# Optimization experiments

Hardware: AMD Instinct MI355X
Metric: run time of the kernel (lower is better)

## Reference

```python
import jax, jax.numpy as jnp
import numpy as np

N, E, F_IN, HID, HEADS, OUT = 50000, 600000, 128, 128, 8, 64
C = HID // HEADS  # per-head channels = 16
NEG_SLOPE = 0.2


def _gat_layer(x, ei_src, ei_dst, Wl, bl, Ws, Wd, a_s, a_d, bc):
    n = x.shape[0]
    lin_out = x @ Wl + bl                              # [N, HID]
    xs = (x @ Ws).reshape(n, HEADS, C)                 # [N, H, C] (lin_src, no bias)
    xd = (x @ Wd).reshape(n, HEADS, C)                 # [N, H, C] (lin_dst, no bias)
    alpha_s = jnp.sum(xs * a_s, axis=-1)               # [N, H]
    alpha_d = jnp.sum(xd * a_d, axis=-1)               # [N, H]
    e = jax.nn.leaky_relu(alpha_s[ei_src] + alpha_d[ei_dst], NEG_SLOPE)  # [E, H]
    # segment softmax over destination nodes
    m = jax.lax.stop_gradient(jax.ops.segment_max(e, ei_dst, num_segments=n))
    p = jnp.exp(e - m[ei_dst])
    denom = jax.ops.segment_sum(p, ei_dst, num_segments=n)
    alpha = p / (denom[ei_dst] + 1e-16)                # [E, H]
    msg = alpha[:, :, None] * xs[ei_src]               # [E, H, C]
    agg = jax.ops.segment_sum(msg, ei_dst, num_segments=n).reshape(n, HID) + bc
    # eval mode: attention/feature dropout are identity
    return jax.nn.elu(lin_out + agg)


def setup_inputs() -> dict:
    key = jax.random.key(0)
    ks = jax.random.split(key, 20)
    s = 0.05
    d = {
        "x": jax.random.normal(ks[0], (N, F_IN), jnp.float32),
        "edge_index": jax.random.randint(ks[1], (2, E), 0, N, jnp.int64)
        if jax.config.jax_enable_x64 else jax.random.randint(ks[1], (2, E), 0, N, jnp.int32),
    }
    dims_in = [F_IN, HID]
    for l in range(2):
        di = dims_in[l]
        d[f"W_lin{l}"] = jax.random.normal(ks[2 + 8 * l], (di, HID), jnp.float32) * s
        d[f"b_lin{l}"] = jnp.zeros((HID,), jnp.float32)
        d[f"W_src{l}"] = jax.random.normal(ks[3 + 8 * l], (di, HID), jnp.float32) * s
        d[f"W_dst{l}"] = jax.random.normal(ks[4 + 8 * l], (di, HID), jnp.float32) * s
        d[f"att_src{l}"] = jax.random.normal(ks[5 + 8 * l], (HEADS, C), jnp.float32) * s
        d[f"att_dst{l}"] = jax.random.normal(ks[6 + 8 * l], (HEADS, C), jnp.float32) * s
        d[f"b_conv{l}"] = jnp.zeros((HID,), jnp.float32)
    d["W_out"] = jax.random.normal(ks[18], (HID, OUT), jnp.float32) * s
    d["b_out"] = jnp.zeros((OUT,), jnp.float32)
    return d


def reference(x, edge_index,
              W_lin0, b_lin0, W_src0, W_dst0, att_src0, att_dst0, b_conv0,
              W_lin1, b_lin1, W_src1, W_dst1, att_src1, att_dst1, b_conv1,
              W_out, b_out):
    ei_src, ei_dst = edge_index[0], edge_index[1]
    h = _gat_layer(x, ei_src, ei_dst, W_lin0, b_lin0, W_src0, W_dst0, att_src0, att_dst0, b_conv0)
    h = _gat_layer(h, ei_src, ei_dst, W_lin1, b_lin1, W_src1, W_dst1, att_src1, att_dst1, b_conv1)
    return h @ W_out + b_out
```

## Files before the change

### kernel.cpp

```cpp
#include <hip/hip_runtime.h>
#include <cstdint>
#include <cstddef>

#define NEG_SLOPE 0.2f

typedef __bf16 bf16x8 __attribute__((ext_vector_type(8)));
typedef float f32x4 __attribute__((ext_vector_type(4)));

static __device__ __forceinline__ unsigned short f2bf(float f) {
  unsigned int u = __float_as_uint(f);
  unsigned int r = (u + 0x7FFFu + ((u >> 16) & 1u)) >> 16;
  return (unsigned short)r;
}
static __device__ __forceinline__ float bf2f(unsigned short u) {
  return __uint_as_float(((unsigned int)u) << 16);
}
static __device__ __forceinline__ float pklo(unsigned int x) {
  return __uint_as_float(x << 16);
}
static __device__ __forceinline__ float pkhi(unsigned int x) {
  return __uint_as_float(x & 0xffff0000u);
}

__global__ void k_degree(const int* __restrict__ ei, int* __restrict__ deg, int E) {
  int e = blockIdx.x * 256 + threadIdx.x;
  if (e < E) atomicAdd(&deg[ei[E + e]], 1);
}

__global__ __launch_bounds__(256) void k_scan_local(const int* __restrict__ deg,
                                                    int* __restrict__ lex,
                                                    int* __restrict__ bsum, int n) {
  __shared__ int ts[256];
  const int t = threadIdx.x;
  const int base = blockIdx.x * 1024 + t * 4;
  int4 d = {0, 0, 0, 0};
  if (base + 3 < n) d = *reinterpret_cast<const int4*>(&deg[base]);
  else {
    if (base + 0 < n) d.x = deg[base + 0];
    if (base + 1 < n) d.y = deg[base + 1];
    if (base + 2 < n) d.z = deg[base + 2];
  }
  int s = d.x + d.y + d.z + d.w;
  ts[t] = s;
  __syncthreads();
  for (int off = 1; off < 256; off <<= 1) {
    int y = (t >= off) ? ts[t - off] : 0;
    __syncthreads();
    ts[t] += y;
    __syncthreads();
  }
  int pre = ts[t] - s;
  int4 o;
  o.x = pre; o.y = pre + d.x; o.z = pre + d.x + d.y; o.w = pre + d.x + d.y + d.z;
  if (base + 3 < n) *reinterpret_cast<int4*>(&lex[base]) = o;
  else {
    if (base + 0 < n) lex[base + 0] = o.x;
    if (base + 1 < n) lex[base + 1] = o.y;
    if (base + 2 < n) lex[base + 2] = o.z;
  }
  if (t == 255) bsum[blockIdx.x] = ts[255];
}

__global__ __launch_bounds__(256) void k_scan_bsum(int* __restrict__ bsum, int nb) {
  __shared__ int ts[256];
  const int t = threadIdx.x;
  int v = (t < nb) ? bsum[t] : 0;
  ts[t] = v;
  __syncthreads();
  for (int off = 1; off < 256; off <<= 1) {
    int y = (t >= off) ? ts[t - off] : 0;
    __syncthreads();
    ts[t] += y;
    __syncthreads();
  }
  if (t < nb) bsum[t] = ts[t] - v;
}

__global__ void k_scan_add(const int* __restrict__ lex, const int* __restrict__ bsum,
                           int* __restrict__ rowptr, int* __restrict__ cursor,
                           int n, int E) {
  int i = blockIdx.x * 256 + threadIdx.x;
  if (i < n) {
    int v = lex[i] + bsum[i >> 10];
    rowptr[i] = v;
    cursor[i] = v;
  }
  if (i == n) rowptr[n] = E;
}

__global__ void k_scatter(const int* __restrict__ ei, int* __restrict__ cursor,
                          unsigned short* __restrict__ col, int E) {
  int e = blockIdx.x * 256 + threadIdx.x;
  if (e >= E) return;
  int d = ei[E + e];
  int pos = atomicAdd(&cursor[d], 1);
  col[pos] = (unsigned short)ei[e];
}

static __device__ __forceinline__ unsigned short pack_wt_elem(
    const float* __restrict__ Wl, const float* __restrict__ Ws,
    const float* __restrict__ Wd, const float* __restrict__ as_,
    const float* __restrict__ ad_, int t) {
  int j = t >> 7, k = t & 127;
  float val;
  if (j < 128) val = Wl[k * 128 + j];
  else if (j < 256) val = Ws[k * 128 + (j - 128)];
  else {
    int jj = j - 256;
    int h = jj & 7;
    const float* W = (jj < 8) ? Ws : Wd;
    const float* a = (jj < 8) ? as_ : ad_;
    float s = 0.f;
#pragma unroll
    for (int c = 0; c < 16; ++c) s += W[k * 128 + h * 16 + c] * a[h * 16 + c];
    val = s;
  }
  return f2bf(val);
}

__global__ void k_pack_all(
    const float* __restrict__ Wl0, const float* __restrict__ Ws0, const float* __restrict__ Wd0,
    const float* __restrict__ as0, const float* __restrict__ ad0,
    const float* __restrict__ Wl1, const float* __restrict__ Ws1, const float* __restrict__ Wd1,
    const float* __restrict__ as1, const float* __restrict__ ad1,
    const float* __restrict__ Wo,
    unsigned short* __restrict__ wt0, unsigned short* __restrict__ wt1,
    unsigned short* __restrict__ wot) {
  const int SZ = 272 * 128;
  int t = blockIdx.x * 256 + threadIdx.x;
  if (t < SZ) {
    wt0[t] = pack_wt_elem(Wl0, Ws0, Wd0, as0, ad0, t);
  } else if (t < 2 * SZ) {
    wt1[t - SZ] = pack_wt_elem(Wl1, Ws1, Wd1, as1, ad1, t - SZ);
  } else if (t < 2 * SZ + 64 * 128) {
    int u = t - 2 * SZ;
    int nn = u >> 7, k = u & 127;
    wot[u] = f2bf(Wo[k * 64 + nn]);
  }
}

template <typename TIN>
__global__ __launch_bounds__(256, 3) void k_gemm_fused(
    const TIN* __restrict__ X, const unsigned short* __restrict__ wt,
    const float* __restrict__ bl, const float* __restrict__ bc,
    unsigned int* __restrict__ ylin_pk, unsigned short* __restrict__ xsb,
    unsigned short* __restrict__ asd_s, unsigned short* __restrict__ asd_d,
    int n) {
  __shared__ __align__(16) unsigned short xa[32][136];
  const int tid = threadIdx.x;
  const int wave = tid >> 6, lane = tid & 63;
  const int lr = lane & 15, lg = lane >> 4;
  const int row0 = blockIdx.x * 32;
  const int f0 = wave * 4;
  const bool w3 = (wave == 3);

  bf16x8 bfr[4][4];
#pragma unroll
  for (int ff = 0; ff < 4; ++ff)
#pragma unroll
    for (int s = 0; s < 4; ++s)
      bfr[ff][s] = *reinterpret_cast<const bf16x8*>(
          &wt[(size_t)((f0 + ff) * 16 + lr) * 128 + s * 32 + lg * 8]);
  bf16x8 bfr4[4];
  if (w3) {
#pragma unroll
    for (int s = 0; s < 4; ++s)
      bfr4[s] = *reinterpret_cast<const bf16x8*>(
          &wt[(size_t)(256 + lr) * 128 + s * 32 + lg * 8]);
  }

  if constexpr (sizeof(TIN) == 4) {
#pragma unroll
    for (int i = 0; i < 4; ++i) {
      int c = tid + i * 256;
      int r = c >> 5, kq = c & 31;
      float4 v = make_float4(0.f, 0.f, 0.f, 0.f);
      if (row0 + r < n)
        v = reinterpret_cast<const float4*>(X)[(size_t)(row0 + r) * 32 + kq];
      ushort4 o;
      o.x = f2bf(v.x); o.y = f2bf(v.y); o.z = f2bf(v.z); o.w = f2bf(v.w);
      *reinterpret_cast<ushort4*>(&xa[r][kq * 4]) = o;
    }
  } else {
#pragma unroll
    for (int i = 0; i < 2; ++i) {
      int c = tid + i * 256;
      int r = c >> 4, ko = c & 15;
      uint4 v = {0u, 0u, 0u, 0u};
      if (row0 + r < n)
        v = reinterpret_cast<const uint4*>(X)[(size_t)(row0 + r) * 16 + ko];
      *reinterpret_cast<uint4*>(&xa[r][ko * 8]) = v;
    }
  }
  __syncthreads();

  f32x4 acc[2][4];
  f32x4 acc4[2];
#pragma unroll
  for (int g = 0; g < 2; ++g) {
    acc4[g] = (f32x4){0.f, 0.f, 0.f, 0.f};
#pragma unroll
    for (int ff = 0; ff < 4; ++ff) acc[g][ff] = (f32x4){0.f, 0.f, 0.f, 0.f};
  }

#pragma unroll
  for (int s = 0; s < 4; ++s) {
    bf16x8 a0 = *reinterpret_cast<const bf16x8*>(&xa[lr][s * 32 + lg * 8]);
    bf16x8 a1 = *reinterpret_cast<const bf16x8*>(&xa[16 + lr][s * 32 + lg * 8]);
#pragma unroll
    for (int ff = 0; ff < 4; ++ff) {
      acc[0][ff] = __builtin_amdgcn_mfma_f32_16x16x32_bf16(a0, bfr[ff][s], acc[0][ff], 0, 0, 0);
      acc[1][ff] = __builtin_amdgcn_mfma_f32_16x16x32_bf16(a1, bfr[ff][s], acc[1][ff], 0, 0, 0);
    }
    if (w3) {
      acc4[0] = __builtin_amdgcn_mfma_f32_16x16x32_bf16(a0, bfr4[s], acc4[0], 0, 0, 0);
      acc4[1] = __builtin_amdgcn_mfma_f32_16x16x32_bf16(a1, bfr4[s], acc4[1], 0, 0, 0);
    }
  }

  if (f0 < 8) {
#pragma unroll
    for (int g = 0; g < 2; ++g)
#pragma unroll
      for (int ff = 0; ff < 4; ++ff) {
        int j = (f0 + ff) * 16 + lr;
        float blc = bl[j] + bc[j];
#pragma unroll
        for (int r = 0; r < 4; ++r) {
          int row = row0 + g * 16 + lg * 4 + r;
          float vb = acc[g][ff][r] + blc;
          float v2 = __shfl(vb, lane ^ 1);
          if (row < n && (lr & 1) == 0)
            ylin_pk[(size_t)row * 64 + (j >> 1)] =
                (unsigned int)f2bf(vb) | ((unsigned int)f2bf(v2) << 16);
        }
      }
  } else {
#pragma unroll
    for (int g = 0; g < 2; ++g)
#pragma unroll
      for (int ff = 0; ff < 4; ++ff) {
        int j = (f0 - 8 + ff) * 16 + lr;
#pragma unroll
        for (int r = 0; r < 4; ++r) {
          int row = row0 + g * 16 + lg * 4 + r;
          if (row < n) xsb[(size_t)row * 128 + j] = f2bf(acc[g][ff][r]);
        }
      }
    if (w3) {
#pragma unroll
      for (int g = 0; g < 2; ++g)
#pragma unroll
        for (int r = 0; r < 4; ++r) {
          int row = row0 + g * 16 + lg * 4 + r;
          if (row < n) {
            unsigned short v = f2bf(acc4[g][r]);
            if (lr < 8) asd_s[(size_t)row * 8 + lr] = v;
            else        asd_d[(size_t)row * 8 + (lr - 8)] = v;
          }
        }
    }
  }
}

__global__ __launch_bounds__(256) void k_gemm_out(
    const unsigned short* __restrict__ X, const unsigned short* __restrict__ wo,
    const float* __restrict__ bias, float* __restrict__ out, int n) {
  __shared__ __align__(16) unsigned short xa[64][136];
  __shared__ __align__(16) unsigned short ws[64][136];
  const int tid = threadIdx.x;
  const int row0 = blockIdx.x * 64;

#pragma unroll
  for (int i = 0; i < 4; ++i) {
    int c = tid + i * 256;
    int r = c >> 4, ko = c & 15;
    uint4 v = {0u, 0u, 0u, 0u};
    if (row0 + r < n)
      v = reinterpret_cast<const uint4*>(X)[(size_t)(row0 + r) * 16 + ko];
    *reinterpret_cast<uint4*>(&xa[r][ko * 8]) = v;
  }
#pragma unroll
  for (int i = 0; i < 4; ++i) {
    int c = tid + i * 256;
    int r = c >> 4, ko = c & 15;
    *reinterpret_cast<uint4*>(&ws[r][ko * 8]) =
        reinterpret_cast<const uint4*>(wo)[(size_t)r * 16 + ko];
  }
  __syncthreads();

  const int w = tid >> 6, lane = tid & 63;
  const int lr = lane & 15, lg = lane >> 4;
  f32x4 acc[4];
#pragma unroll
  for (int f = 0; f < 4; ++f) acc[f] = (f32x4){0.f, 0.f, 0.f, 0.f};

#pragma unroll
  for (int s = 0; s < 4; ++s) {
    bf16x8 a = *reinterpret_cast<const bf16x8*>(&xa[w * 16 + lr][s * 32 + lg * 8]);
#pragma unroll
    for (int f = 0; f < 4; ++f) {
      bf16x8 b = *reinterpret_cast<const bf16x8*>(&ws[f * 16 + lr][s * 32 + lg * 8]);
      acc[f] = __builtin_amdgcn_mfma_f32_16x16x32_bf16(a, b, acc[f], 0, 0, 0);
    }
  }
#pragma unroll
  for (int f = 0; f < 4; ++f) {
#pragma unroll
    for (int r = 0; r < 4; ++r) {
      int row = row0 + w * 16 + lg * 4 + r;
      if (row < n)
        out[(size_t)row * 64 + f * 16 + lr] = acc[f][r] + bias[f * 16 + lr];
    }
  }
}

__global__ __launch_bounds__(256) void k_aggregate(
    const unsigned int* __restrict__ ylin_pk, const unsigned int* __restrict__ xsp,
    const unsigned short* __restrict__ asd_s, const unsigned short* __restrict__ asd_d,
    const int* __restrict__ rowptr, const unsigned short* __restrict__ col,
    unsigned int* __restrict__ hout_pk, int n) {
  int node = (blockIdx.x * blockDim.x + threadIdx.x) >> 6;
  if (node >= n) return;
  const int lane = threadIdx.x & 63;
  const int el = lane >> 3;
  const int hh = lane & 7;
  const int hb4 = (lane >> 3) << 2;
  const int beg = rowptr[node], end = rowptr[node + 1];

  const float ad_hh = bf2f(asd_d[(size_t)node * 8 + hh]);

  float dsum = 0.f, acc0 = 0.f, acc1 = 0.f;
  int ebase = beg;
  for (; ebase + 8 < end; ebase += 16) {
    int eA = ebase + el;
    int eB = ebase + 8 + el;
    bool vB = eB < end;
    int esB = vB ? eB : (end - 1);
    int srcA = (int)__builtin_nontemporal_load(&col[eA]);
    int srcB = (int)__builtin_nontemporal_load(&col[esB]);
    float svA = bf2f(asd_s[(size_t)srcA * 8 + hh]) + ad_hh;
    float svB = bf2f(asd_s[(size_t)srcB * 8 + hh]) + ad_hh;
    svA = fmaxf(svA, NEG_SLOPE * svA);
    svB = fmaxf(svB, NEG_SLOPE * svB);
    float peA = __expf(svA);
    float peB = vB ? __expf(svB) : 0.f;
#pragma unroll
    for (int q = 0; q < 8; ++q) {
      float pq = __uint_as_float(__builtin_amdgcn_ds_bpermute(
          q * 32 + hb4, __float_as_uint(peA)));
      int sq = __builtin_amdgcn_readlane(srcA, q * 8);
      unsigned int xv = xsp[(size_t)sq * 64 + lane];
      dsum += pq;
      acc0 += pq * pklo(xv);
      acc1 += pq * pkhi(xv);
    }
#pragma unroll
    for (int q = 0; q < 8; ++q) {
      float pq = __uint_as_float(__builtin_amdgcn_ds_bpermute(
          q * 32 + hb4, __float_as_uint(peB)));
      int sq = __builtin_amdgcn_readlane(srcB, q * 8);
      unsigned int xv = xsp[(size_t)sq * 64 + lane];
      dsum += pq;
      acc0 += pq * pklo(xv);
      acc1 += pq * pkhi(xv);
    }
  }
  for (; ebase < end; ebase += 8) {
    int e1 = ebase + el;
    bool valid = e1 < end;
    int esafe = valid ? e1 : (end - 1);
    int srcp = (int)__builtin_nontemporal_load(&col[esafe]);
    float sv = bf2f(asd_s[(size_t)srcp * 8 + hh]) + ad_hh;
    sv = fmaxf(sv, NEG_SLOPE * sv);
    float pe = valid ? __expf(sv) : 0.f;
#pragma unroll
    for (int q = 0; q < 8; ++q) {
      float pq = __uint_as_float(__builtin_amdgcn_ds_bpermute(
          q * 32 + hb4, __float_as_uint(pe)));
      int sq = __builtin_amdgcn_readlane(srcp, q * 8);
      unsigned int xv = xsp[(size_t)sq * 64 + lane];
      dsum += pq;
      acc0 += pq * pklo(xv);
      acc1 += pq * pkhi(xv);
    }
  }
  float inv = 1.f / (dsum + 1e-16f);
  unsigned int y = __builtin_nontemporal_load(&ylin_pk[(size_t)node * 64 + lane]);
  float l0 = pklo(y) + acc0 * inv;
  float l1 = pkhi(y) + acc1 * inv;
  l0 = l0 > 0.f ? l0 : __expf(l0) - 1.f;
  l1 = l1 > 0.f ? l1 : __expf(l1) - 1.f;
  hout_pk[(size_t)node * 64 + lane] =
      (unsigned int)f2bf(l0) | ((unsigned int)f2bf(l1) << 16);
}

extern "C" void kernel_launch(void* const* d_in, const int* in_sizes, int n_in,
                              void* d_out, int out_size, void* d_ws, size_t ws_size,
                              hipStream_t stream) {
  const float* x      = (const float*)d_in[0];
  const int*   ei     = (const int*)d_in[1];
  const float* W_lin0 = (const float*)d_in[2];
  const float* b_lin0 = (const float*)d_in[3];
  const float* W_src0 = (const float*)d_in[4];
  const float* W_dst0 = (const float*)d_in[5];
  const float* att_s0 = (const float*)d_in[6];
  const float* att_d0 = (const float*)d_in[7];
  const float* b_cnv0 = (const float*)d_in[8];
  const float* W_lin1 = (const float*)d_in[9];
  const float* b_lin1 = (const float*)d_in[10];
  const float* W_src1 = (const float*)d_in[11];
  const float* W_dst1 = (const float*)d_in[12];
  const float* att_s1 = (const float*)d_in[13];
  const float* att_d1 = (const float*)d_in[14];
  const float* b_cnv1 = (const float*)d_in[15];
  const float* W_out  = (const float*)d_in[16];
  const float* b_out  = (const float*)d_in[17];
  float* out = (float*)d_out;

  const int N = in_sizes[0] / 128;
  const int E = in_sizes[1] / 2;
  const int NB = (N + 1023) / 1024;
  const int MB32 = (N + 31) / 32;

  char* p = (char*)d_ws;
  unsigned int* ylin    = (unsigned int*)p;   p += (size_t)N * 64 * 4;
  unsigned short* xsb   = (unsigned short*)p; p += (size_t)N * 128 * 2;
  unsigned short* hb    = (unsigned short*)p; p += (size_t)N * 128 * 2;
  unsigned short* asd_s = (unsigned short*)p; p += (size_t)N * 8 * 2;
  unsigned short* asd_d = (unsigned short*)p; p += (size_t)N * 8 * 2;
  unsigned short* wt0   = (unsigned short*)p; p += (size_t)272 * 128 * 2;
  unsigned short* wt1   = (unsigned short*)p; p += (size_t)272 * 128 * 2;
  unsigned short* wot   = (unsigned short*)p; p += (size_t)64 * 128 * 2;
  int* rowptr = (int*)p;                      p += (size_t)(N + 4) * 4;
  int* cursor = (int*)p;                      p += (size_t)N * 4;
  int* deg    = (int*)p;                      p += (size_t)N * 4;
  int* lex    = (int*)p;                      p += (size_t)N * 4;
  int* bsum   = (int*)p;                      p += (size_t)256 * 4;
  unsigned short* col = (unsigned short*)p;   p += (size_t)E * 2;

  dim3 b256(256);

  hipMemsetAsync(deg, 0, (size_t)N * 4, stream);
  k_degree<<<(E + 255) / 256, b256, 0, stream>>>(ei, deg, E);
  k_scan_local<<<NB, b256, 0, stream>>>(deg, lex, bsum, N);
  k_scan_bsum<<<1, b256, 0, stream>>>(bsum, NB);
  k_scan_add<<<(N + 256) / 256, b256, 0, stream>>>(lex, bsum, rowptr, cursor, N, E);
  k_scatter<<<(E + 255) / 256, b256, 0, stream>>>(ei, cursor, col, E);

  k_pack_all<<<(2 * 272 * 128 + 64 * 128 + 255) / 256, b256, 0, stream>>>(
      W_lin0, W_src0, W_dst0, att_s0, att_d0,
      W_lin1, W_src1, W_dst1, att_s1, att_d1,
      W_out, wt0, wt1, wot);

  for (int layer = 0; layer < 2; ++layer) {
    const float* bl = layer ? b_lin1 : b_lin0;
    const float* bc = layer ? b_cnv1 : b_cnv0;
    const unsigned short* wt = layer ? wt1 : wt0;

    if (layer == 0)
      k_gemm_fused<float><<<MB32, b256, 0, stream>>>(x, wt0, bl, bc, ylin, xsb,
                                                     asd_s, asd_d, N);
    else
      k_gemm_fused<unsigned short><<<MB32, b256, 0, stream>>>(hb, wt, bl, bc, ylin, xsb,
                                                              asd_s, asd_d, N);
    k_aggregate<<<(N + 3) / 4, b256, 0, stream>>>(
        ylin, (const unsigned int*)xsb, asd_s, asd_d, rowptr, col,
        (unsigned int*)hb, N);
  }
  k_gemm_out<<<(N + 63) / 64, b256, 0, stream>>>(hb, wot, b_out, out, N);
}
```

Before: 187.1 us.

## Merge preprocessing kernels and interleave edge scatter with layer-0 GEMM blocks

Weight packing and degree counting are merged into one launch. The CSR scatter is folded into the layer-0 GEMM kernel, with scatter blocks spread evenly among GEMM blocks. This cuts launch count and lets the atomic-bound scatter overlap tensor-core work. The output GEMM now keeps its weights in registers and uses 32-row tiles with no weight LDS staging, and the ylin load in aggregate is issued earlier to hide its latency. Interleaving heterogeneous blocks may hurt occupancy balance, and the scatter's col ordering still depends on atomics.

```diff
diff --git a/kernel.cpp b/kernel.cpp
--- a/kernel.cpp
+++ b/kernel.cpp
@@ -20,11 +20,6 @@
 }
 static __device__ __forceinline__ float pkhi(unsigned int x) {
   return __uint_as_float(x & 0xffff0000u);
-}
-
-__global__ void k_degree(const int* __restrict__ ei, int* __restrict__ deg, int E) {
-  int e = blockIdx.x * 256 + threadIdx.x;
-  if (e < E) atomicAdd(&deg[ei[E + e]], 1);
 }
 
 __global__ __launch_bounds__(256) void k_scan_local(const int* __restrict__ deg,
@@ -86,15 +81,6 @@
     cursor[i] = v;
   }
   if (i == n) rowptr[n] = E;
-}
-
-__global__ void k_scatter(const int* __restrict__ ei, int* __restrict__ cursor,
-                          unsigned short* __restrict__ col, int E) {
-  int e = blockIdx.x * 256 + threadIdx.x;
-  if (e >= E) return;
-  int d = ei[E + e];
-  int pos = atomicAdd(&cursor[d], 1);
-  col[pos] = (unsigned short)ei[e];
 }
 
 static __device__ __forceinline__ unsigned short pack_wt_elem(
@@ -118,30 +104,162 @@
   return f2bf(val);
 }
 
-__global__ void k_pack_all(
+__global__ void k_init(
     const float* __restrict__ Wl0, const float* __restrict__ Ws0, const float* __restrict__ Wd0,
     const float* __restrict__ as0, const float* __restrict__ ad0,
     const float* __restrict__ Wl1, const float* __restrict__ Ws1, const float* __restrict__ Wd1,
     const float* __restrict__ as1, const float* __restrict__ ad1,
     const float* __restrict__ Wo,
     unsigned short* __restrict__ wt0, unsigned short* __restrict__ wt1,
-    unsigned short* __restrict__ wot) {
+    unsigned short* __restrict__ wot,
+    const int* __restrict__ ei, int* __restrict__ deg, int E, int packBlocks) {
   const int SZ = 272 * 128;
-  int t = blockIdx.x * 256 + threadIdx.x;
-  if (t < SZ) {
-    wt0[t] = pack_wt_elem(Wl0, Ws0, Wd0, as0, ad0, t);
-  } else if (t < 2 * SZ) {
-    wt1[t - SZ] = pack_wt_elem(Wl1, Ws1, Wd1, as1, ad1, t - SZ);
-  } else if (t < 2 * SZ + 64 * 128) {
-    int u = t - 2 * SZ;
-    int nn = u >> 7, k = u & 127;
-    wot[u] = f2bf(Wo[k * 64 + nn]);
-  }
-}
-
-template <typename TIN>
-__global__ __launch_bounds__(256, 3) void k_gemm_fused(
-    const TIN* __restrict__ X, const unsigned short* __restrict__ wt,
+  if ((int)blockIdx.x < packBlocks) {
+    int t = blockIdx.x * 256 + threadIdx.x;
+    if (t < SZ) {
+      wt0[t] = pack_wt_elem(Wl0, Ws0, Wd0, as0, ad0, t);
+    } else if (t < 2 * SZ) {
+      wt1[t - SZ] = pack_wt_elem(Wl1, Ws1, Wd1, as1, ad1, t - SZ);
+    } else if (t < 2 * SZ + 64 * 128) {
+      int u = t - 2 * SZ;
+      int nn = u >> 7, k = u & 127;
+      wot[u] = f2bf(Wo[k * 64 + nn]);
+    }
+  } else {
+    int e = (blockIdx.x - packBlocks) * 256 + threadIdx.x;
+    if (e < E) atomicAdd(&deg[ei[E + e]], 1);
+  }
+}
+
+__global__ __launch_bounds__(256, 3) void k_gemm0_scatter(
+    const float* __restrict__ X, const unsigned short* __restrict__ wt,
+    const float* __restrict__ bl, const float* __restrict__ bc,
+    unsigned int* __restrict__ ylin_pk, unsigned short* __restrict__ xsb,
+    unsigned short* __restrict__ asd_s, unsigned short* __restrict__ asd_d,
+    int n, int gemmBlocks,
+    const int* __restrict__ ei, int* __restrict__ cursor,
+    unsigned short* __restrict__ col, int E, int total) {
+  __shared__ __align__(16) unsigned short xa[32][136];
+  const int i = blockIdx.x;
+  const int before = (int)(((long long)i * gemmBlocks) / total);
+  const int after  = (int)(((long long)(i + 1) * gemmBlocks) / total);
+
+  if (after == before) {
+    int e = (i - after) * 256 + threadIdx.x;
+    if (e < E) {
+      int d = ei[E + e];
+      int pos = atomicAdd(&cursor[d], 1);
+      col[pos] = (unsigned short)ei[e];
+    }
+    return;
+  }
+
+  const int tid = threadIdx.x;
+  const int wave = tid >> 6, lane = tid & 63;
+  const int lr = lane & 15, lg = lane >> 4;
+  const int row0 = before * 32;
+  const int f0 = wave * 4;
+  const bool w3 = (wave == 3);
+
+  bf16x8 bfr[4][4];
+#pragma unroll
+  for (int ff = 0; ff < 4; ++ff)
+#pragma unroll
+    for (int s = 0; s < 4; ++s)
+      bfr[ff][s] = *reinterpret_cast<const bf16x8*>(
+          &wt[(size_t)((f0 + ff) * 16 + lr) * 128 + s * 32 + lg * 8]);
+  bf16x8 bfr4[4];
+  if (w3) {
+#pragma unroll
+    for (int s = 0; s < 4; ++s)
+      bfr4[s] = *reinterpret_cast<const bf16x8*>(
+          &wt[(size_t)(256 + lr) * 128 + s * 32 + lg * 8]);
+  }
+
+#pragma unroll
+  for (int ii = 0; ii < 4; ++ii) {
+    int c = tid + ii * 256;
+    int r = c >> 5, kq = c & 31;
+    float4 v = make_float4(0.f, 0.f, 0.f, 0.f);
+    if (row0 + r < n)
+      v = reinterpret_cast<const float4*>(X)[(size_t)(row0 + r) * 32 + kq];
+    ushort4 o;
+    o.x = f2bf(v.x); o.y = f2bf(v.y); o.z = f2bf(v.z); o.w = f2bf(v.w);
+    *reinterpret_cast<ushort4*>(&xa[r][kq * 4]) = o;
+  }
+  __syncthreads();
+
+  f32x4 acc[2][4];
+  f32x4 acc4[2];
+#pragma unroll
+  for (int g = 0; g < 2; ++g) {
+    acc4[g] = (f32x4){0.f, 0.f, 0.f, 0.f};
+#pragma unroll
+    for (int ff = 0; ff < 4; ++ff) acc[g][ff] = (f32x4){0.f, 0.f, 0.f, 0.f};
+  }
+
+#pragma unroll
+  for (int s = 0; s < 4; ++s) {
+    bf16x8 a0 = *reinterpret_cast<const bf16x8*>(&xa[lr][s * 32 + lg * 8]);
+    bf16x8 a1 = *reinterpret_cast<const bf16x8*>(&xa[16 + lr][s * 32 + lg * 8]);
+#pragma unroll
+    for (int ff = 0; ff < 4; ++ff) {
+      acc[0][ff] = __builtin_amdgcn_mfma_f32_16x16x32_bf16(a0, bfr[ff][s], acc[0][ff], 0, 0, 0);
+      acc[1][ff] = __builtin_amdgcn_mfma_f32_16x16x32_bf16(a1, bfr[ff][s], acc[1][ff], 0, 0, 0);
+    }
+    if (w3) {
+      acc4[0] = __builtin_amdgcn_mfma_f32_16x16x32_bf16(a0, bfr4[s], acc4[0], 0, 0, 0);
+      acc4[1] = __builtin_amdgcn_mfma_f32_16x16x32_bf16(a1, bfr4[s], acc4[1], 0, 0, 0);
+    }
+  }
+
+  if (f0 < 8) {
+#pragma unroll
+    for (int g = 0; g < 2; ++g)
+#pragma unroll
+      for (int ff = 0; ff < 4; ++ff) {
+        int j = (f0 + ff) * 16 + lr;
+        float blc = bl[j] + bc[j];
+#pragma unroll
+        for (int r = 0; r < 4; ++r) {
+          int row = row0 + g * 16 + lg * 4 + r;
+          float vb = acc[g][ff][r] + blc;
+          float v2 = __shfl(vb, lane ^ 1);
+          if (row < n && (lr & 1) == 0)
+            ylin_pk[(size_t)row * 64 + (j >> 1)] =
+                (unsigned int)f2bf(vb) | ((unsigned int)f2bf(v2) << 16);
+        }
+      }
+  } else {
+#pragma unroll
+    for (int g = 0; g < 2; ++g)
+#pragma unroll
+      for (int ff = 0; ff < 4; ++ff) {
+        int j = (f0 - 8 + ff) * 16 + lr;
+#pragma unroll
+        for (int r = 0; r < 4; ++r) {
+          int row = row0 + g * 16 + lg * 4 + r;
+          if (row < n) xsb[(size_t)row * 128 + j] = f2bf(acc[g][ff][r]);
+        }
+      }
+    if (w3) {
+#pragma unroll
+      for (int g = 0; g < 2; ++g)
+#pragma unroll
+        for (int r = 0; r < 4; ++r) {
+          int row = row0 + g * 16 + lg * 4 + r;
+          if (row < n) {
+            unsigned short v = f2bf(acc4[g][r]);
+            if (lr < 8) asd_s[(size_t)row * 8 + lr] = v;
+            else        asd_d[(size_t)row * 8 + (lr - 8)] = v;
+          }
+        }
+    }
+  }
+}
+
+__global__ __launch_bounds__(256, 3) void k_gemm_fused1(
+    const unsigned short* __restrict__ X, const unsigned short* __restrict__ wt,
     const float* __restrict__ bl, const float* __restrict__ bc,
     unsigned int* __restrict__ ylin_pk, unsigned short* __restrict__ xsb,
     unsigned short* __restrict__ asd_s, unsigned short* __restrict__ asd_d,
@@ -169,28 +287,14 @@
           &wt[(size_t)(256 + lr) * 128 + s * 32 + lg * 8]);
   }
 
-  if constexpr (sizeof(TIN) == 4) {
-#pragma unroll
-    for (int i = 0; i < 4; ++i) {
-      int c = tid + i * 256;
-      int r = c >> 5, kq = c & 31;
-      float4 v = make_float4(0.f, 0.f, 0.f, 0.f);
-      if (row0 + r < n)
-        v = reinterpret_cast<const float4*>(X)[(size_t)(row0 + r) * 32 + kq];
-      ushort4 o;
-      o.x = f2bf(v.x); o.y = f2bf(v.y); o.z = f2bf(v.z); o.w = f2bf(v.w);
-      *reinterpret_cast<ushort4*>(&xa[r][kq * 4]) = o;
-    }
-  } else {
-#pragma unroll
-    for (int i = 0; i < 2; ++i) {
-      int c = tid + i * 256;
-      int r = c >> 4, ko = c & 15;
-      uint4 v = {0u, 0u, 0u, 0u};
-      if (row0 + r < n)
-        v = reinterpret_cast<const uint4*>(X)[(size_t)(row0 + r) * 16 + ko];
-      *reinterpret_cast<uint4*>(&xa[r][ko * 8]) = v;
-    }
+#pragma unroll
+  for (int i = 0; i < 2; ++i) {
+    int c = tid + i * 256;
+    int r = c >> 4, ko = c & 15;
+    uint4 v = {0u, 0u, 0u, 0u};
+    if (row0 + r < n)
+      v = reinterpret_cast<const uint4*>(X)[(size_t)(row0 + r) * 16 + ko];
+    *reinterpret_cast<uint4*>(&xa[r][ko * 8]) = v;
   }
   __syncthreads();
 
@@ -263,16 +367,23 @@
   }
 }
 
-__global__ __launch_bounds__(256) void k_gemm_out(
-    const unsigned short* __restrict__ X, const unsigned short* __restrict__ wo,
+__global__ __launch_bounds__(256, 3) void k_gemm_out(
+    const unsigned short* __restrict__ X, const unsigned short* __restrict__ wot,
     const float* __restrict__ bias, float* __restrict__ out, int n) {
-  __shared__ __align__(16) unsigned short xa[64][136];
-  __shared__ __align__(16) unsigned short ws[64][136];
+  __shared__ __align__(16) unsigned short xa[32][136];
   const int tid = threadIdx.x;
-  const int row0 = blockIdx.x * 64;
-
-#pragma unroll
-  for (int i = 0; i < 4; ++i) {
+  const int wave = tid >> 6, lane = tid & 63;
+  const int lr = lane & 15, lg = lane >> 4;
+  const int row0 = blockIdx.x * 32;
+
+  bf16x8 bo[4];
+#pragma unroll
+  for (int s = 0; s < 4; ++s)
+    bo[s] = *reinterpret_cast<const bf16x8*>(
+        &wot[(size_t)(wave * 16 + lr) * 128 + s * 32 + lg * 8]);
+
+#pragma unroll
+  for (int i = 0; i < 2; ++i) {
     int c = tid + i * 256;
     int r = c >> 4, ko = c & 15;
     uint4 v = {0u, 0u, 0u, 0u};
@@ -280,39 +391,26 @@
       v = reinterpret_cast<const uint4*>(X)[(size_t)(row0 + r) * 16 + ko];
     *reinterpret_cast<uint4*>(&xa[r][ko * 8]) = v;
   }
-#pragma unroll
-  for (int i = 0; i < 4; ++i) {
-    int c = tid + i * 256;
-    int r = c >> 4, ko = c & 15;
-    *reinterpret_cast<uint4*>(&ws[r][ko * 8]) =
-        reinterpret_cast<const uint4*>(wo)[(size_t)r * 16 + ko];
-  }
   __syncthreads();
 
-  const int w = tid >> 6, lane = tid & 63;
-  const int lr = lane & 15, lg = lane >> 4;
-  f32x4 acc[4];
-#pragma unroll
-  for (int f = 0; f < 4; ++f) acc[f] = (f32x4){0.f, 0.f, 0.f, 0.f};
-
+  f32x4 acc[2];
+  acc[0] = (f32x4){0.f, 0.f, 0.f, 0.f};
+  acc[1] = (f32x4){0.f, 0.f, 0.f, 0.f};
 #pragma unroll
   for (int s = 0; s < 4; ++s) {
-    bf16x8 a = *reinterpret_cast<const bf16x8*>(&xa[w * 16 + lr][s * 32 + lg * 8]);
-#pragma unroll
-    for (int f = 0; f < 4; ++f) {
-      bf16x8 b = *reinterpret_cast<const bf16x8*>(&ws[f * 16 + lr][s * 32 + lg * 8]);
-      acc[f] = __builtin_amdgcn_mfma_f32_16x16x32_bf16(a, b, acc[f], 0, 0, 0);
-    }
-  }
-#pragma unroll
-  for (int f = 0; f < 4; ++f) {
+    bf16x8 a0 = *reinterpret_cast<const bf16x8*>(&xa[lr][s * 32 + lg * 8]);
+    bf16x8 a1 = *reinterpret_cast<const bf16x8*>(&xa[16 + lr][s * 32 + lg * 8]);
+    acc[0] = __builtin_amdgcn_mfma_f32_16x16x32_bf16(a0, bo[s], acc[0], 0, 0, 0);
+    acc[1] = __builtin_amdgcn_mfma_f32_16x16x32_bf16(a1, bo[s], acc[1], 0, 0, 0);
+  }
+  float bv = bias[wave * 16 + lr];
+#pragma unroll
+  for (int g = 0; g < 2; ++g)
 #pragma unroll
     for (int r = 0; r < 4; ++r) {
-      int row = row0 + w * 16 + lg * 4 + r;
-      if (row < n)
-        out[(size_t)row * 64 + f * 16 + lr] = acc[f][r] + bias[f * 16 + lr];
-    }
-  }
+      int row = row0 + g * 16 + lg * 4 + r;
+      if (row < n) out[(size_t)row * 64 + wave * 16 + lr] = acc[g][r] + bv;
+    }
 }
 
 __global__ __launch_bounds__(256) void k_aggregate(
@@ -329,6 +427,7 @@
   const int beg = rowptr[node], end = rowptr[node + 1];
 
   const float ad_hh = bf2f(asd_d[(size_t)node * 8 + hh]);
+  unsigned int y = __builtin_nontemporal_load(&ylin_pk[(size_t)node * 64 + lane]);
 
   float dsum = 0.f, acc0 = 0.f, acc1 = 0.f;
   int ebase = beg;
@@ -386,7 +485,6 @@
     }
   }
   float inv = 1.f / (dsum + 1e-16f);
-  unsigned int y = __builtin_nontemporal_load(&ylin_pk[(size_t)node * 64 + lane]);
   float l0 = pklo(y) + acc0 * inv;
   float l1 = pkhi(y) + acc1 * inv;
   l0 = l0 > 0.f ? l0 : __expf(l0) - 1.f;
@@ -422,6 +520,8 @@
   const int E = in_sizes[1] / 2;
   const int NB = (N + 1023) / 1024;
   const int MB32 = (N + 31) / 32;
+  const int SB = (E + 255) / 256;
+  const int PACKB = (2 * 272 * 128 + 64 * 128 + 255) / 256;
 
   char* p = (char*)d_ws;
   unsigned int* ylin    = (unsigned int*)p;   p += (size_t)N * 64 * 4;
@@ -442,31 +542,25 @@
   dim3 b256(256);
 
   hipMemsetAsync(deg, 0, (size_t)N * 4, stream);
-  k_degree<<<(E + 255) / 256, b256, 0, stream>>>(ei, deg, E);
+  k_init<<<PACKB + SB, b256, 0, stream>>>(
+      W_lin0, W_src0, W_dst0, att_s0, att_d0,
+      W_lin1, W_src1, W_dst1, att_s1, att_d1,
+      W_out, wt0, wt1, wot, ei, deg, E, PACKB);
   k_scan_local<<<NB, b256, 0, stream>>>(deg, lex, bsum, N);
   k_scan_bsum<<<1, b256, 0, stream>>>(bsum, NB);
   k_scan_add<<<(N + 256) / 256, b256, 0, stream>>>(lex, bsum, rowptr, cursor, N, E);
-  k_scatter<<<(E + 255) / 256, b256, 0, stream>>>(ei, cursor, col, E);
-
-  k_pack_all<<<(2 * 272 * 128 + 64 * 128 + 255) / 256, b256, 0, stream>>>(
-      W_lin0, W_src0, W_dst0, att_s0, att_d0,
-      W_lin1, W_src1, W_dst1, att_s1, att_d1,
-      W_out, wt0, wt1, wot);
-
-  for (int layer = 0; layer < 2; ++layer) {
-    const float* bl = layer ? b_lin1 : b_lin0;
-    const float* bc = layer ? b_cnv1 : b_cnv0;
-    const unsigned short* wt = layer ? wt1 : wt0;
-
-    if (layer == 0)
-      k_gemm_fused<float><<<MB32, b256, 0, stream>>>(x, wt0, bl, bc, ylin, xsb,
-                                                     asd_s, asd_d, N);
-    else
-      k_gemm_fused<unsigned short><<<MB32, b256, 0, stream>>>(hb, wt, bl, bc, ylin, xsb,
-                                                              asd_s, asd_d, N);
-    k_aggregate<<<(N + 3) / 4, b256, 0, stream>>>(
-        ylin, (const unsigned int*)xsb, asd_s, asd_d, rowptr, col,
-        (unsigned int*)hb, N);
-  }
-  k_gemm_out<<<(N + 63) / 64, b256, 0, stream>>>(hb, wot, b_out, out, N);
-}
+
+  k_gemm0_scatter<<<MB32 + SB, b256, 0, stream>>>(
+      x, wt0, b_lin0, b_cnv0, ylin, xsb, asd_s, asd_d, N, MB32,
+      ei, cursor, col, E, MB32 + SB);
+
+  k_aggregate<<<(N + 3) / 4, b256, 0, stream>>>(
+      ylin, (const unsigned int*)xsb, asd_s, asd_d, rowptr, col,
+      (unsigned int*)hb, N);
+  k_gemm_fused1<<<MB32, b256, 0, stream>>>(hb, wt1, b_lin1, b_cnv1,
+                                           ylin, xsb, asd_s, asd_d, N);
+  k_aggregate<<<(N + 3) / 4, b256, 0, stream>>>(
+      ylin, (const unsigned int*)xsb, asd_s, asd_d, rowptr, col,
+      (unsigned int*)hb, N);
+  k_gemm_out<<<MB32, b256, 0, stream>>>(hb, wot, b_out, out, N);
+}
```

Result: faster. 165.3 us (-11.7%).
